# Kernel optimization log

Hardware: AMD Instinct MI355X
Metric: run time of the kernel (lower is better)

## Reference

```python
import jax, jax.numpy as jnp
import numpy as np

B, S, E, H = 4, 2048, 512, 8
DK = E // H  # 64 quantum wires per head


def setup_inputs() -> dict:
    key = jax.random.key(0)
    k1, k2, k3, k4 = jax.random.split(key, 4)
    x = jax.random.normal(k1, (B, S, E), dtype=jnp.float32)
    theta = jax.random.normal(k2, (DK,), dtype=jnp.float32)
    W = jax.random.normal(k3, (E, E), dtype=jnp.float32) * (1.0 / np.sqrt(E))
    b = jax.random.normal(k4, (E,), dtype=jnp.float32) * 0.01
    return {"x": x, "theta": theta, "W": W, "b": b}


def _quantum_project(x, theta):
    # x: [B,S,E] -> heads [B,H,S,DK]. Circuit per wire: RX(x_i) then RX(theta_i),
    # product state => <Z_i> = cos(x_i + theta_i).
    xh = x.reshape(B, S, H, DK).transpose(0, 2, 1, 3)  # [B,H,S,DK]
    return jnp.cos(xh + theta)


def reference(x, theta, W, b):
    q = _quantum_project(x, theta)
    k = _quantum_project(x, theta)
    v = _quantum_project(x, theta)
    scores = jnp.einsum('bhqd,bhkd->bhqk', q, k) / jnp.sqrt(jnp.float32(DK))
    attn = jax.nn.softmax(scores, axis=-1)  # dropout is identity in eval
    out = jnp.einsum('bhqk,bhkd->bhqd', attn, v)  # [B,H,S,DK]
    out = out.transpose(0, 2, 1, 3).reshape(B, S, E)
    return out @ W.T + b
```

## Files before the change

### kernel.cpp

```cpp
#include <hip/hip_runtime.h>
#include <hip/hip_bf16.h>
#include <math.h>

#define B_ 4
#define S_ 2048
#define E_ 512
#define H_ 8
#define DK_ 64

typedef __attribute__((ext_vector_type(8))) short short8;
typedef __attribute__((ext_vector_type(4))) float f32x4;
typedef _Float16 half8 __attribute__((ext_vector_type(8)));
typedef _Float16 half4 __attribute__((ext_vector_type(4)));
typedef __fp16 fp16x2 __attribute__((ext_vector_type(2)));
typedef unsigned uint4v __attribute__((ext_vector_type(4)));

__device__ inline short8 ld8(const void* p) {
  return *reinterpret_cast<const short8*>(p);
}
__device__ inline half8 ld8h(const void* p) {
  return *reinterpret_cast<const half8*>(p);
}

static __device__ inline unsigned pk2(float a, float b) {
  fp16x2 h = __builtin_amdgcn_cvt_pkrtz(a, b);
  return __builtin_bit_cast(unsigned, h);
}
static __device__ inline half8 pack8(float p0, float p1, float p2, float p3,
                                     float p4, float p5, float p6, float p7) {
  uint4v u;
  u[0] = pk2(p0, p1); u[1] = pk2(p2, p3);
  u[2] = pk2(p4, p5); u[3] = pk2(p6, p7);
  return __builtin_bit_cast(half8, u);
}


__global__ __launch_bounds__(256) void prep_g_kernel(
    const float* __restrict__ x, const float* __restrict__ theta,
    const float* __restrict__ W, _Float16* __restrict__ kA,
    _Float16* __restrict__ vA, _Float16* __restrict__ wb) {
  const int tid = threadIdx.x;

  if (blockIdx.y == B_ * H_) {
    const int base = (blockIdx.x * 256 + tid) * 8;
#pragma unroll
    for (int it = 0; it < 4; ++it) {
      const int i = base + it * 65536;
      float4 a = *reinterpret_cast<const float4*>(W + i);
      float4 c = *reinterpret_cast<const float4*>(W + i + 4);
      half8 v;
      v[0]=(_Float16)a.x; v[1]=(_Float16)a.y; v[2]=(_Float16)a.z; v[3]=(_Float16)a.w;
      v[4]=(_Float16)c.x; v[5]=(_Float16)c.y; v[6]=(_Float16)c.z; v[7]=(_Float16)c.w;
      *reinterpret_cast<half8*>(wb + i) = v;
    }
    return;
  }

  const int bh = blockIdx.y;
  const int b = bh >> 3, h = bh & 7;
  const int s0 = blockIdx.x * 64;
  const int wave = tid >> 6, lane = tid & 63;
  const int col = lane & 15, quad = lane >> 4;
  __shared__ _Float16 tile[64 * 72];

  const float* xp = x + ((size_t)(b * S_ + s0)) * E_ + h * DK_;
  const int dc4 = (tid & 15) * 4;
  const float4 th = *reinterpret_cast<const float4*>(theta + dc4);
#pragma unroll
  for (int it = 0; it < 4; ++it) {
    const int sr = it * 16 + (tid >> 4);
    float4 xv = *reinterpret_cast<const float4*>(xp + (size_t)sr * E_ + dc4);
    half4 hv;
    hv[0] = (_Float16)__cosf(xv.x + th.x);
    hv[1] = (_Float16)__cosf(xv.y + th.y);
    hv[2] = (_Float16)__cosf(xv.z + th.z);
    hv[3] = (_Float16)__cosf(xv.w + th.w);
    *reinterpret_cast<half4*>(tile + sr * 72 + dc4) = hv;
  }
  __syncthreads();

  _Float16* kb = kA + (size_t)bh * (S_ * DK_);
  _Float16* vb = vA + (size_t)bh * (S_ * DK_);
  const int Gbase = s0 >> 5;
#pragma unroll
  for (int it2 = 0; it2 < 2; ++it2) {
    int c = wave + it2 * 4;
    int Gl = c >> 2, g = (c >> 1) & 1, hh = c & 1;
    int ploc = Gl * 32 + ((col >> 2) << 3) + g * 4 + (col & 3);
    half8 v = ld8h(tile + ploc * 72 + hh * 32 + quad * 8);
    *reinterpret_cast<half8*>(
        kb + ((size_t)(Gbase + Gl) * 2048 + (g * 2 + hh) * 512 + lane * 8)) = v;
  }
#pragma unroll
  for (int it2 = 0; it2 < 2; ++it2) {
    int c = wave + it2 * 4;
    int Gl = c >> 2, dcc = c & 3;
    half8 v;
#pragma unroll
    for (int j = 0; j < 8; ++j)
      v[j] = tile[(Gl * 32 + quad * 8 + j) * 72 + dcc * 16 + col];
    *reinterpret_cast<half8*>(
        vb + ((size_t)(Gbase + Gl) * 2048 + dcc * 512 + lane * 8)) = v;
  }
}

__global__ __launch_bounds__(256, 3) void attn_kernel(
    const _Float16* __restrict__ kA, const _Float16* __restrict__ vA,
    _Float16* __restrict__ ao) {
  const int tid = threadIdx.x;
  const int wave = tid >> 6, lane = tid & 63;
  const int col = lane & 15, quad = lane >> 4;
  const int wg = blockIdx.x + 32 * blockIdx.y;
  const int xcd = wg & 7, slot = wg >> 3;
  const int bh = xcd * 4 + (slot >> 5);
  const int q0 = (slot & 31) * 64;
  const _Float16* kb = kA + (size_t)bh * (S_ * DK_);
  const _Float16* vb = vA + (size_t)bh * (S_ * DK_);

  const _Float16 hC1 = (_Float16)0.18033688011112042f;
  half8 qa[4][2];
#pragma unroll
  for (int qc = 0; qc < 4; ++qc)
#pragma unroll
    for (int hh = 0; hh < 2; ++hh)
      qa[qc][hh] = ld8h(kb + (size_t)((q0 >> 5) + (qc >> 1)) * 2048 +
                        ((qc & 1) * 2 + hh) * 512 + lane * 8) * hC1;

  const half8 kOnes = {(_Float16)1, (_Float16)1, (_Float16)1, (_Float16)1,
                       (_Float16)1, (_Float16)1, (_Float16)1, (_Float16)1};

  f32x4 o[4][4];
  f32x4 ol[4];
#pragma unroll
  for (int qc = 0; qc < 4; ++qc) {
#pragma unroll
    for (int dc = 0; dc < 4; ++dc) o[qc][dc] = f32x4{0.f, 0.f, 0.f, 0.f};
    ol[qc] = f32x4{0.f, 0.f, 0.f, 0.f};
  }

  const _Float16* kw = kb + (size_t)wave * 16 * 2048 + lane * 8;
  const _Float16* vw = vb + (size_t)wave * 16 * 2048 + lane * 8;

  for (int it = 0; it < 16; ++it) {
    const _Float16* kit = kw + it * 2048;
    const _Float16* vit = vw + it * 2048;
    half8 kf00 = ld8h(kit);
    half8 kf01 = ld8h(kit + 512);
    half8 kf10 = ld8h(kit + 1024);
    half8 kf11 = ld8h(kit + 1536);
    half8 vf0 = ld8h(vit);
    half8 vf1 = ld8h(vit + 512);
    half8 vf2 = ld8h(vit + 1024);
    half8 vf3 = ld8h(vit + 1536);

#pragma unroll
    for (int qc = 0; qc < 4; ++qc) {
      f32x4 z0{0.f, 0.f, 0.f, 0.f}, z1{0.f, 0.f, 0.f, 0.f};
      __builtin_amdgcn_s_setprio(1);
      z0 = __builtin_amdgcn_mfma_f32_16x16x32_f16(kf00, qa[qc][0], z0, 0, 0, 0);
      z0 = __builtin_amdgcn_mfma_f32_16x16x32_f16(kf01, qa[qc][1], z0, 0, 0, 0);
      z1 = __builtin_amdgcn_mfma_f32_16x16x32_f16(kf10, qa[qc][0], z1, 0, 0, 0);
      z1 = __builtin_amdgcn_mfma_f32_16x16x32_f16(kf11, qa[qc][1], z1, 0, 0, 0);
      __builtin_amdgcn_s_setprio(0);
      float p0 = __builtin_amdgcn_exp2f(z0[0]);
      float p1 = __builtin_amdgcn_exp2f(z0[1]);
      float p2 = __builtin_amdgcn_exp2f(z0[2]);
      float p3 = __builtin_amdgcn_exp2f(z0[3]);
      float p4 = __builtin_amdgcn_exp2f(z1[0]);
      float p5 = __builtin_amdgcn_exp2f(z1[1]);
      float p6 = __builtin_amdgcn_exp2f(z1[2]);
      float p7 = __builtin_amdgcn_exp2f(z1[3]);
      half8 pf = pack8(p0, p1, p2, p3, p4, p5, p6, p7);
      __builtin_amdgcn_s_setprio(1);
      o[qc][0] = __builtin_amdgcn_mfma_f32_16x16x32_f16(vf0, pf, o[qc][0], 0, 0, 0);
      o[qc][1] = __builtin_amdgcn_mfma_f32_16x16x32_f16(vf1, pf, o[qc][1], 0, 0, 0);
      o[qc][2] = __builtin_amdgcn_mfma_f32_16x16x32_f16(vf2, pf, o[qc][2], 0, 0, 0);
      o[qc][3] = __builtin_amdgcn_mfma_f32_16x16x32_f16(vf3, pf, o[qc][3], 0, 0, 0);
      ol[qc] = __builtin_amdgcn_mfma_f32_16x16x32_f16(kOnes, pf, ol[qc], 0, 0, 0);
      __builtin_amdgcn_s_setprio(0);
    }
  }

  __shared__ float reds[8192];
  if (quad == 0) {
#pragma unroll
    for (int qc = 0; qc < 4; ++qc) reds[(wave * 4 + qc) * 16 + col] = ol[qc][0];
  }
  __syncthreads();
  float ltot = 0.f;
#pragma unroll
  for (int w2 = 0; w2 < 4; ++w2) ltot += reds[(w2 * 4 + wave) * 16 + col];
  float inv = __builtin_amdgcn_rcpf(ltot);

  const int b = bh >> 3, h = bh & 7;
  const int qrow = q0 + ((wave >> 1) << 5) + ((col >> 2) << 3) + (wave & 1) * 4 + (col & 3);
  _Float16* op = ao + ((size_t)b * S_ + qrow) * E_ + h * DK_;
  __syncthreads();
#pragma unroll
  for (int qp = 0; qp < 2; ++qp) {
    if (qp) __syncthreads();
#pragma unroll
    for (int hh = 0; hh < 2; ++hh)
#pragma unroll
      for (int dc = 0; dc < 4; ++dc)
        *reinterpret_cast<f32x4*>(reds + hh * 4096 + wave * 1024 + lane * 16 + dc * 4) =
            o[qp * 2 + hh][dc];
    __syncthreads();
    if ((wave >> 1) == qp) {
      const float* rp = reds + (wave & 1) * 4096;
#pragma unroll
      for (int dc = 0; dc < 4; ++dc) {
        f32x4 acc = *reinterpret_cast<const f32x4*>(rp + lane * 16 + dc * 4);
#pragma unroll
        for (int w2 = 1; w2 < 4; ++w2)
          acc = acc + *reinterpret_cast<const f32x4*>(rp + w2 * 1024 + lane * 16 + dc * 4);
        half4 pk4;
        pk4[0] = (_Float16)(acc[0] * inv);
        pk4[1] = (_Float16)(acc[1] * inv);
        pk4[2] = (_Float16)(acc[2] * inv);
        pk4[3] = (_Float16)(acc[3] * inv);
        *reinterpret_cast<half4*>(op + dc * 16 + quad * 4) = pk4;
      }
    }
  }
}

__global__ __launch_bounds__(256, 4) void proj_kernel(
    const _Float16* __restrict__ ao, const _Float16* __restrict__ wb,
    const float* __restrict__ bias, float* __restrict__ out) {
  const int tid = threadIdx.x;
  const int wave = tid >> 6, lane = tid & 63;
  const int col = lane & 15, quad = lane >> 4;
  const int wg = blockIdx.x + 128 * blockIdx.y;
  const int xcd = wg & 7, slot = wg >> 3;
  const int m0 = (xcd * 16 + (slot >> 3)) * 64;
  const int n0 = (slot & 7) * 64;
  __shared__ short at[64 * 136];
  __shared__ short bt[64 * 136];

  const int srw = tid >> 4;
  const int soff = (tid & 15) * 8;

  short8 ap_[4], wp_[4];
#pragma unroll
  for (int it = 0; it < 4; ++it) {
    int row = it * 16 + srw;
    ap_[it] = ld8(ao + (size_t)(m0 + row) * E_ + soff);
    wp_[it] = ld8(wb + (size_t)(n0 + row) * E_ + soff);
  }

  f32x4 acc[4] = {{0.f,0.f,0.f,0.f},{0.f,0.f,0.f,0.f},{0.f,0.f,0.f,0.f},{0.f,0.f,0.f,0.f}};

  for (int k0 = 0; k0 < E_; k0 += 128) {
#pragma unroll
    for (int it = 0; it < 4; ++it) {
      int row = it * 16 + srw;
      *reinterpret_cast<short8*>(at + row * 136 + soff) = ap_[it];
      *reinterpret_cast<short8*>(bt + row * 136 + soff) = wp_[it];
    }
    __syncthreads();
    if (k0 + 128 < E_) {
#pragma unroll
      for (int it = 0; it < 4; ++it) {
        int row = it * 16 + srw;
        ap_[it] = ld8(ao + (size_t)(m0 + row) * E_ + k0 + 128 + soff);
        wp_[it] = ld8(wb + (size_t)(n0 + row) * E_ + k0 + 128 + soff);
      }
    }
#pragma unroll
    for (int ks = 0; ks < 4; ++ks) {
      half8 a = *reinterpret_cast<const half8*>(at + (wave * 16 + col) * 136 + ks * 32 + quad * 8);
#pragma unroll
      for (int f = 0; f < 4; ++f) {
        half8 bb = *reinterpret_cast<const half8*>(bt + (f * 16 + col) * 136 + ks * 32 + quad * 8);
        acc[f] = __builtin_amdgcn_mfma_f32_16x16x32_f16(a, bb, acc[f], 0, 0, 0);
      }
    }
    __syncthreads();
  }

#pragma unroll
  for (int f = 0; f < 4; ++f) {
    float bv = bias[n0 + f * 16 + col];
#pragma unroll
    for (int r = 0; r < 4; ++r) {
      int row = m0 + wave * 16 + quad * 4 + r;
      out[(size_t)row * E_ + n0 + f * 16 + col] = acc[f][r] + bv;
    }
  }
}

extern "C" void kernel_launch(void* const* d_in, const int* in_sizes, int n_in,
                              void* d_out, int out_size, void* d_ws, size_t ws_size,
                              hipStream_t stream) {
  const float* x = (const float*)d_in[0];
  const float* theta = (const float*)d_in[1];
  const float* W = (const float*)d_in[2];
  const float* bias = (const float*)d_in[3];
  float* out = (float*)d_out;
  char* ws = (char*)d_ws;
  const size_t gsz = (size_t)B_ * H_ * S_ * DK_ * 2;
  _Float16* kA = (_Float16*)ws;
  _Float16* vA = (_Float16*)(ws + gsz);
  _Float16* ao = (_Float16*)(ws + 2 * gsz);
  _Float16* wb = (_Float16*)(ws + 3 * gsz);

  prep_g_kernel<<<dim3(S_ / 64, B_ * H_ + 1), 256, 0, stream>>>(x, theta, W, kA, vA, wb);
  attn_kernel<<<dim3(S_ / 64, B_ * H_), 256, 0, stream>>>(kA, vA, ao);
  proj_kernel<<<dim3((B_ * S_) / 64, E_ / 64), 256, 0, stream>>>(ao, wb, bias, out);
}
```

Measured before the change: 124.0 us.

## Split attention KV range across two waves instead of four per block

Attention blocks shrink from 4 waves to 2 waves, with each wave covering twice as many key/value chunks (32 iterations instead of 16). The cross-wave reduction of row sums and output accumulators is rewritten for 2 waves, and the shared reduction buffer shrinks accordingly. The intent is to cut LDS reduction traffic and barrier overhead per block and to lower the shared-memory footprint, which may allow more resident blocks. The cost is a longer serial KV loop per wave and fewer waves per block available to hide latency.

```diff
diff --git a/kernel.cpp b/kernel.cpp
--- a/kernel.cpp
+++ b/kernel.cpp
@@ -104,7 +104,7 @@
   }
 }
 
-__global__ __launch_bounds__(256, 3) void attn_kernel(
+__global__ __launch_bounds__(128, 3) void attn_kernel(
     const _Float16* __restrict__ kA, const _Float16* __restrict__ vA,
     _Float16* __restrict__ ao) {
   const int tid = threadIdx.x;
@@ -138,10 +138,10 @@
     ol[qc] = f32x4{0.f, 0.f, 0.f, 0.f};
   }
 
-  const _Float16* kw = kb + (size_t)wave * 16 * 2048 + lane * 8;
-  const _Float16* vw = vb + (size_t)wave * 16 * 2048 + lane * 8;
-
-  for (int it = 0; it < 16; ++it) {
+  const _Float16* kw = kb + (size_t)wave * 32 * 2048 + lane * 8;
+  const _Float16* vw = vb + (size_t)wave * 32 * 2048 + lane * 8;
+
+  for (int it = 0; it < 32; ++it) {
     const _Float16* kit = kw + it * 2048;
     const _Float16* vit = vw + it * 2048;
     half8 kf00 = ld8h(kit);
@@ -181,44 +181,42 @@
     }
   }
 
-  __shared__ float reds[8192];
+  __shared__ float reds[2048];
   if (quad == 0) {
 #pragma unroll
     for (int qc = 0; qc < 4; ++qc) reds[(wave * 4 + qc) * 16 + col] = ol[qc][0];
   }
   __syncthreads();
-  float ltot = 0.f;
-#pragma unroll
-  for (int w2 = 0; w2 < 4; ++w2) ltot += reds[(w2 * 4 + wave) * 16 + col];
-  float inv = __builtin_amdgcn_rcpf(ltot);
+  float ltotA = reds[(0 * 4 + wave) * 16 + col] + reds[(1 * 4 + wave) * 16 + col];
+  float ltotB = reds[(0 * 4 + wave + 2) * 16 + col] + reds[(1 * 4 + wave + 2) * 16 + col];
+  float invA = __builtin_amdgcn_rcpf(ltotA);
+  float invB = __builtin_amdgcn_rcpf(ltotB);
 
   const int b = bh >> 3, h = bh & 7;
-  const int qrow = q0 + ((wave >> 1) << 5) + ((col >> 2) << 3) + (wave & 1) * 4 + (col & 3);
-  _Float16* op = ao + ((size_t)b * S_ + qrow) * E_ + h * DK_;
+  const int qrowA = q0 + ((col >> 2) << 3) + wave * 4 + (col & 3);
+  const int qrowB = qrowA + 32;
+  _Float16* opA = ao + ((size_t)b * S_ + qrowA) * E_ + h * DK_;
+  _Float16* opB = ao + ((size_t)b * S_ + qrowB) * E_ + h * DK_;
   __syncthreads();
 #pragma unroll
-  for (int qp = 0; qp < 2; ++qp) {
-    if (qp) __syncthreads();
-#pragma unroll
-    for (int hh = 0; hh < 2; ++hh)
-#pragma unroll
-      for (int dc = 0; dc < 4; ++dc)
-        *reinterpret_cast<f32x4*>(reds + hh * 4096 + wave * 1024 + lane * 16 + dc * 4) =
-            o[qp * 2 + hh][dc];
+  for (int p = 0; p < 4; ++p) {
+    if (p) __syncthreads();
+#pragma unroll
+    for (int dc = 0; dc < 4; ++dc)
+      *reinterpret_cast<f32x4*>(reds + wave * 1024 + lane * 16 + dc * 4) = o[p][dc];
     __syncthreads();
-    if ((wave >> 1) == qp) {
-      const float* rp = reds + (wave & 1) * 4096;
+    if (wave == (p & 1)) {
+      float invv = (p < 2) ? invA : invB;
+      _Float16* op = (p < 2) ? opA : opB;
 #pragma unroll
       for (int dc = 0; dc < 4; ++dc) {
-        f32x4 acc = *reinterpret_cast<const f32x4*>(rp + lane * 16 + dc * 4);
-#pragma unroll
-        for (int w2 = 1; w2 < 4; ++w2)
-          acc = acc + *reinterpret_cast<const f32x4*>(rp + w2 * 1024 + lane * 16 + dc * 4);
+        f32x4 acc = *reinterpret_cast<const f32x4*>(reds + lane * 16 + dc * 4);
+        acc = acc + *reinterpret_cast<const f32x4*>(reds + 1024 + lane * 16 + dc * 4);
         half4 pk4;
-        pk4[0] = (_Float16)(acc[0] * inv);
-        pk4[1] = (_Float16)(acc[1] * inv);
-        pk4[2] = (_Float16)(acc[2] * inv);
-        pk4[3] = (_Float16)(acc[3] * inv);
+        pk4[0] = (_Float16)(acc[0] * invv);
+        pk4[1] = (_Float16)(acc[1] * invv);
+        pk4[2] = (_Float16)(acc[2] * invv);
+        pk4[3] = (_Float16)(acc[3] * invv);
         *reinterpret_cast<half4*>(op + dc * 16 + quad * 4) = pk4;
       }
     }
@@ -306,6 +304,6 @@
   _Float16* wb = (_Float16*)(ws + 3 * gsz);
 
   prep_g_kernel<<<dim3(S_ / 64, B_ * H_ + 1), 256, 0, stream>>>(x, theta, W, kA, vA, wb);
-  attn_kernel<<<dim3(S_ / 64, B_ * H_), 256, 0, stream>>>(kA, vA, ao);
+  attn_kernel<<<dim3(32, 32), 128, 0, stream>>>(kA, vA, ao);
   proj_kernel<<<dim3((B_ * S_) / 64, E_ / 64), 256, 0, stream>>>(ao, wb, bias, out);
 }
```

Result: faster. 120.8 us (median of 2 runs) (-2.6%).
